# Kernel tuning notes

Hardware: AMD Instinct MI355X
Metric: run time of the kernel (lower is better)

Reference implementation:

```python
import jax, jax.numpy as jnp
import numpy as np

NUM_HEADS = 12
HEAD_CH = 64
WINDOW = 4


def _relative_to_absolute(x):
    # x: (B, H, L, 2L-1) -> (B, H, L, L) via skew trick
    B, H, L, _ = x.shape
    x = jnp.pad(x, ((0, 0), (0, 0), (0, 0), (0, 1)))        # (B,H,L,2L)
    x = x.reshape(B, H, L * 2 * L)
    x = jnp.pad(x, ((0, 0), (0, 0), (0, L - 1)))
    x = x.reshape(B, H, L + 1, 2 * L - 1)
    return x[:, :, :L, L - 1:]


def _get_relative_embeddings(emb, L):
    # emb: (H, 2W+1, D) -> (H, 2L-1, D)
    pad = max(0, L - WINDOW - 1)
    start = max(0, WINDOW - L + 1)
    e = jnp.pad(emb, ((0, 0), (pad, pad), (0, 0)))
    return e[:, start:start + 2 * L - 1, :]


def _forward(x, wq, bq, wk, bk, wv, bv, wo, bo, emb_rel_k, emb_rel_v):
    B, C, L = x.shape
    H, D = NUM_HEADS, HEAD_CH
    scale = 1.0 / np.sqrt(D).astype(np.float32)

    # 1x1 conv == channel matmul
    q = jnp.einsum('oc,bcl->bol', wq, x) + bq[None, :, None]
    k = jnp.einsum('oc,bcl->bol', wk, x) + bk[None, :, None]
    v = jnp.einsum('oc,bcl->bol', wv, x) + bv[None, :, None]

    # (B, C, L) -> (B, H, L, D)
    q = q.reshape(B, H, D, L).transpose(0, 1, 3, 2)
    k = k.reshape(B, H, D, L).transpose(0, 1, 3, 2)
    v = v.reshape(B, H, D, L).transpose(0, 1, 3, 2)

    score = jnp.einsum('bhld,bhmd->bhlm', q, k) * scale      # (B,H,L,L)

    rel_k = _get_relative_embeddings(emb_rel_k, L)           # (H, 2L-1, D)
    s_rel = jnp.einsum('bhld,hmd->bhlm', q, rel_k)           # (B,H,L,2L-1)
    score = score + _relative_to_absolute(s_rel) * scale

    attn = jax.nn.softmax(score, axis=-1)                    # dropout p=0 -> identity

    res = jnp.einsum('bhlm,bhmd->bhld', attn, v)             # (B,H,L,D)

    # absolute_to_relative skew
    a = jnp.pad(attn, ((0, 0), (0, 0), (0, 0), (0, L - 1)))
    a = a.reshape(B, H, L * (2 * L - 1))
    a = jnp.pad(a, ((0, 0), (0, 0), (L, 0)))
    rel_w = a.reshape(B, H, L, 2 * L)[:, :, :, 1:]           # (B,H,L,2L-1)

    rel_v = _get_relative_embeddings(emb_rel_v, L)           # (H, 2L-1, D)
    res = res + jnp.einsum('bhlm,hmd->bhld', rel_w, rel_v)

    res = res.transpose(0, 1, 3, 2).reshape(B, H * D, L)     # (B, C, L)
    out = jnp.einsum('oc,bcl->bol', wo, res) + bo[None, :, None]
    return out


def setup_inputs() -> dict:
    key = jax.random.key(0)
    ks = jax.random.split(key, 11)
    B, C, L = 4, 768, 1024
    rel_std = HEAD_CH ** (-0.5)
    xavier = np.sqrt(6.0 / (C + C)).astype(np.float32)
    return {
        'x': jax.random.normal(ks[0], (B, C, L), jnp.float32),
        'wq': jax.random.uniform(ks[1], (C, C), jnp.float32, -xavier, xavier),
        'bq': jnp.zeros((C,), jnp.float32),
        'wk': jax.random.uniform(ks[2], (C, C), jnp.float32, -xavier, xavier),
        'bk': jnp.zeros((C,), jnp.float32),
        'wv': jax.random.uniform(ks[3], (C, C), jnp.float32, -xavier, xavier),
        'bv': jnp.zeros((C,), jnp.float32),
        'wo': jax.random.normal(ks[4], (C, C), jnp.float32) * 0.02,
        'bo': jnp.zeros((C,), jnp.float32),
        'emb_rel_k': jax.random.normal(ks[5], (NUM_HEADS, 2 * WINDOW + 1, HEAD_CH), jnp.float32) * rel_std,
        'emb_rel_v': jax.random.normal(ks[6], (NUM_HEADS, 2 * WINDOW + 1, HEAD_CH), jnp.float32) * rel_std,
    }


def reference(x, wq, bq, wk, bk, wv, bv, wo, bo, emb_rel_k, emb_rel_v):
    return _forward(x, wq, bq, wk, bk, wv, bv, wo, bo, emb_rel_k, emb_rel_v)
```

## Files before the change

kernel.cpp:

```cpp
#include <hip/hip_runtime.h>

#define NB   4
#define NH   12
#define HD   64
#define CCH  768
#define LQ   1024
#define SCALE 0.125f
#define STAB  4.0f
#define WELE (CCH*CCH)

typedef unsigned short u16;
typedef __bf16 bf16x8 __attribute__((ext_vector_type(8)));
typedef unsigned short u16x8 __attribute__((ext_vector_type(8)));
typedef unsigned short u16x4 __attribute__((ext_vector_type(4)));
typedef float floatx4 __attribute__((ext_vector_type(4)));
typedef float floatx16 __attribute__((ext_vector_type(16)));

__device__ __forceinline__ float bf2f(u16 u) {
    union { unsigned int i; float f; } x; x.i = ((unsigned int)u) << 16; return x.f;
}
__device__ __forceinline__ u16 f2bf_u(float f) {
    union { float f; unsigned int i; } x; x.f = f;
    unsigned int i = x.i;
    return (u16)((i + 0x7FFFu + ((i >> 16) & 1u)) >> 16);
}
__device__ __forceinline__ void glds16(const u16* g, u16* l) {
    __builtin_amdgcn_global_load_lds(
        (const __attribute__((address_space(1))) unsigned int*)g,
        (__attribute__((address_space(3))) unsigned int*)l, 16, 0, 0);
}

__global__ __launch_bounds__(256) void convert_w_kernel(
    const float* __restrict__ wq, const float* __restrict__ wk,
    const float* __restrict__ wv, const float* __restrict__ wo,
    u16* __restrict__ wb)
{
    const int p = blockIdx.y;
    const float* src = (p == 0) ? wq : (p == 1) ? wk : (p == 2) ? wv : wo;
    u16* dst = wb + (size_t)p * WELE;
    const int idx = (blockIdx.x * 256 + threadIdx.x) * 4;
    const float4 v = *reinterpret_cast<const float4*>(src + idx);
    u16x4 o;
    o[0] = f2bf_u(v.x); o[1] = f2bf_u(v.y); o[2] = f2bf_u(v.z); o[3] = f2bf_u(v.w);
    *reinterpret_cast<u16x4*>(dst + idx) = o;
}

__global__ __launch_bounds__(256) void transpose_x_kernel(
    const float* __restrict__ x, u16* __restrict__ xT)
{
    __shared__ u16 tile[64 * 68];
    const int l0 = blockIdx.x * 64, c0 = blockIdx.y * 64, b = blockIdx.z;
    const int t = threadIdx.x;
    const float* xb = x + (size_t)b * CCH * LQ;
    {
        const int l = t & 63, cg = t >> 6;
        for (int i = 0; i < 16; ++i) {
            const int c = cg * 16 + i;
            tile[c * 68 + l] = f2bf_u(xb[(size_t)(c0 + c) * LQ + l0 + l]);
        }
    }
    __syncthreads();
    {
        const int c = t & 63, lg = t >> 6;
        for (int i = 0; i < 16; ++i) {
            const int l = lg * 16 + i;
            xT[((size_t)b * LQ + l0 + l) * CCH + c0 + c] = tile[c * 68 + l];
        }
    }
}

#define GEMM_CORE(Ag, Bg)                                                     \
    __shared__ __align__(16) u16 a_tile[128 * 64];                            \
    __shared__ __align__(16) u16 b_tile[128 * 64];                            \
    const int t = threadIdx.x;                                                \
    const int wave = t >> 6, lane = t & 63;                                   \
    const int quad = lane >> 4, l16 = lane & 15;                              \
    const int wm = (wave >> 1) * 64, wn = (wave & 1) * 64;                    \
    floatx4 acc[4][4];                                                        \
    _Pragma("unroll") for (int mi = 0; mi < 4; ++mi)                          \
        _Pragma("unroll") for (int ni = 0; ni < 4; ++ni)                      \
            _Pragma("unroll") for (int r = 0; r < 4; ++r) acc[mi][ni][r] = 0.f;\
    for (int k0 = 0; k0 < CCH; k0 += 64) {                                    \
        __syncthreads();                                                      \
        _Pragma("unroll") for (int i = 0; i < 4; ++i) {                       \
            const int sbase = wave * 256 + i * 64;                            \
            const int s = sbase + lane;                                       \
            const int m = s >> 3, pos = s & 7;                                \
            const int gpos = pos ^ (m & 7);                                   \
            glds16(Ag + (size_t)(m0 + m) * CCH + k0 + gpos * 8,               \
                   &a_tile[sbase * 8]);                                       \
            glds16(Bg + (size_t)(n0 + m) * CCH + k0 + gpos * 8,               \
                   &b_tile[sbase * 8]);                                       \
        }                                                                     \
        __syncthreads();                                                      \
        bf16x8 af[2][4], bfr[2][4];                                           \
        _Pragma("unroll") for (int s = 0; s < 2; ++s)                         \
            _Pragma("unroll") for (int i = 0; i < 4; ++i) {                   \
                const int am = wm + i * 16 + l16;                             \
                const int bn = wn + i * 16 + l16;                             \
                const int c = s * 4 + quad;                                   \
                af[s][i]  = *reinterpret_cast<const bf16x8*>(                 \
                    &a_tile[(am * 8 + (c ^ (am & 7))) * 8]);                  \
                bfr[s][i] = *reinterpret_cast<const bf16x8*>(                 \
                    &b_tile[(bn * 8 + (c ^ (bn & 7))) * 8]);                  \
            }                                                                 \
        _Pragma("unroll") for (int s = 0; s < 2; ++s)                         \
            _Pragma("unroll") for (int mi = 0; mi < 4; ++mi)                  \
                _Pragma("unroll") for (int ni = 0; ni < 4; ++ni)              \
                    acc[mi][ni] = __builtin_amdgcn_mfma_f32_16x16x32_bf16(    \
                        af[s][mi], bfr[s][ni], acc[mi][ni], 0, 0, 0);         \
    }

__global__ __launch_bounds__(256) void proj_qk_kernel(
    const u16* __restrict__ xT, const u16* __restrict__ wb,
    const float* __restrict__ bq, const float* __restrict__ bk,
    u16* __restrict__ Qlc, u16* __restrict__ Klc)
{
    const int z = blockIdx.z, b = z >> 1, p = z & 1;
    const int n0 = blockIdx.x * 128, m0 = blockIdx.y * 128;
    const u16* Ag = xT + (size_t)b * LQ * CCH;
    const u16* Bg = wb + (size_t)p * WELE;
    const float* bias = (p == 0) ? bq : bk;
    u16* Y = ((p == 0) ? Qlc : Klc) + (size_t)b * LQ * CCH;

    GEMM_CORE(Ag, Bg)

#pragma unroll
    for (int ni = 0; ni < 4; ++ni) {
        const int o = n0 + wn + ni * 16 + l16;
        const float bb = bias[o];
#pragma unroll
        for (int mi = 0; mi < 4; ++mi)
#pragma unroll
            for (int r = 0; r < 4; ++r) {
                const int l = m0 + wm + mi * 16 + quad * 4 + r;
                Y[(size_t)l * CCH + o] = f2bf_u(acc[mi][ni][r] + bb);
            }
    }
}

__global__ __launch_bounds__(256) void proj_v_kernel(
    const u16* __restrict__ xT, const u16* __restrict__ wb,
    const float* __restrict__ bv, u16* __restrict__ Vw)
{
    const int b = blockIdx.z;
    const int n0 = blockIdx.x * 128, m0 = blockIdx.y * 128;
    const u16* Ag = wb + (size_t)2 * WELE;
    const u16* Bg = xT + (size_t)b * LQ * CCH;
    u16* Y = Vw + (size_t)b * CCH * LQ;

    GEMM_CORE(Ag, Bg)

#pragma unroll
    for (int mi = 0; mi < 4; ++mi) {
#pragma unroll
        for (int r = 0; r < 4; ++r) {
            const int o = m0 + wm + mi * 16 + quad * 4 + r;
            const float bb = bv[o];
#pragma unroll
            for (int ni = 0; ni < 4; ++ni) {
                const int l = n0 + wn + ni * 16 + l16;
                Y[(size_t)o * LQ + l] = f2bf_u(acc[mi][ni][r] + bb);
            }
        }
    }
}

__global__ __launch_bounds__(256) void proj_out_kernel(
    const u16* __restrict__ resb, const u16* __restrict__ wb,
    const float* __restrict__ bo, float* __restrict__ out)
{
    const int b = blockIdx.z;
    const int n0 = blockIdx.x * 128, m0 = blockIdx.y * 128;
    const u16* Ag = wb + (size_t)3 * WELE;
    const u16* Bg = resb + (size_t)b * LQ * CCH;
    float* Y = out + (size_t)b * CCH * LQ;

    GEMM_CORE(Ag, Bg)

#pragma unroll
    for (int mi = 0; mi < 4; ++mi) {
#pragma unroll
        for (int r = 0; r < 4; ++r) {
            const int o = m0 + wm + mi * 16 + quad * 4 + r;
            const float bb = bo[o];
#pragma unroll
            for (int ni = 0; ni < 4; ++ni) {
                const int l = n0 + wn + ni * 16 + l16;
                Y[(size_t)o * LQ + l] = acc[mi][ni][r] + bb;
            }
        }
    }
}

#define KSTRIDE 72
#define PSTR 40

__global__ __launch_bounds__(256) void attn_kernel(
    const u16* __restrict__ Qlc, const u16* __restrict__ Klc,
    const u16* __restrict__ Vw,
    const float* __restrict__ erk, const float* __restrict__ erv,
    u16* __restrict__ resb)
{
    __shared__ __align__(16) u16 kv_lds[2 * 64 * KSTRIDE];
    __shared__ __align__(16) u16 p_lds[4 * 32 * PSTR];
    __shared__ float bias_lds[64 * 9];
    __shared__ float bandw_lds[64 * 9];
    __shared__ float erk_lds[9 * 64];
    __shared__ float erv_lds[9 * 64];
    __shared__ float l_red[64];

    u16* k16 = kv_lds;
    u16* v16 = kv_lds + 64 * KSTRIDE;
    float* ored = (float*)kv_lds;
    u16* kdiag = kv_lds;

    const int t = threadIdx.x;
    const int wave = t >> 6, lane = t & 63;
    const int hw = lane >> 5, l32 = lane & 31;
    const int qh = wave & 1, kh = wave >> 1;
    const int l0 = blockIdx.x * 64, h = blockIdx.y, b = blockIdx.z;

    const u16* Qb = Qlc + (size_t)b * LQ * CCH + h * HD;
    const u16* Kb = Klc + (size_t)b * LQ * CCH + h * HD;
    const u16* Vb = Vw + ((size_t)b * CCH + h * HD) * LQ;

    for (int i = t; i < 9 * 64; i += 256) {
        erk_lds[i] = erk[(size_t)h * 9 * 64 + i];
        erv_lds[i] = erv[(size_t)h * 9 * 64 + i];
    }

    const int qrow = qh * 32 + l32;
    const int lgq = l0 + qrow;

    bf16x8 qa[4];
#pragma unroll
    for (int c = 0; c < 4; ++c)
        qa[c] = *reinterpret_cast<const bf16x8*>(&Qb[(size_t)lgq * CCH + c * 16 + hw * 8]);

    __syncthreads();

    if (kh == 0) {
        float qf[32];
#pragma unroll
        for (int c = 0; c < 4; ++c) {
            union { bf16x8 v; u16x8 u; } a; a.v = qa[c];
#pragma unroll
            for (int j = 0; j < 8; ++j) qf[c * 8 + j] = bf2f(a.u[j]);
        }
        for (int dl = 0; dl < 9; ++dl) {
            float s = 0.f;
#pragma unroll
            for (int c = 0; c < 4; ++c)
#pragma unroll
                for (int j = 0; j < 8; ++j)
                    s += qf[c * 8 + j] * erk_lds[dl * 64 + c * 16 + hw * 8 + j];
            s += __shfl_xor(s, 32, 64);
            if (hw == 0) bias_lds[qrow * 9 + dl] = s;
        }
    }

    floatx16 O[2];
#pragma unroll
    for (int dt = 0; dt < 2; ++dt)
#pragma unroll
        for (int r = 0; r < 16; ++r) O[dt][r] = 0.f;
    float l_acc = 0.f;

    u16* pw = p_lds + wave * 32 * PSTR;

    for (int kb = 0; kb < 16; ++kb) {
        const int j0 = kb * 64;
        __syncthreads();
        {
            const int j = t >> 2, seg = t & 3;
            const u16x8* ks = reinterpret_cast<const u16x8*>(&Kb[(size_t)(j0 + j) * CCH + seg * 16]);
            *reinterpret_cast<u16x8*>(&k16[j * KSTRIDE + seg * 16])     = ks[0];
            *reinterpret_cast<u16x8*>(&k16[j * KSTRIDE + seg * 16 + 8]) = ks[1];
            const u16x8* vs = reinterpret_cast<const u16x8*>(&Vb[(size_t)j * LQ + j0 + seg * 16]);
            *reinterpret_cast<u16x8*>(&v16[j * KSTRIDE + seg * 16])     = vs[0];
            *reinterpret_cast<u16x8*>(&v16[j * KSTRIDE + seg * 16 + 8]) = vs[1];
        }
        __syncthreads();

        floatx16 sc;
#pragma unroll
        for (int r = 0; r < 16; ++r) sc[r] = 0.f;
#pragma unroll
        for (int c = 0; c < 4; ++c) {
            const bf16x8 ka = *reinterpret_cast<const bf16x8*>(
                &k16[(kh * 32 + l32) * KSTRIDE + c * 16 + hw * 8]);
            sc = __builtin_amdgcn_mfma_f32_32x32x16_bf16(ka, qa[c], sc, 0, 0, 0);
        }

        const int kbase = j0 + kh * 32;
        if (kbase + 31 >= l0 + qh * 32 - 4 && kbase <= l0 + qh * 32 + 35) {
#pragma unroll
            for (int r = 0; r < 16; ++r) {
                const int key = kbase + (r & 3) + 8 * (r >> 2) + 4 * hw;
                const int delta = key - lgq + 4;
                if (delta >= 0 && delta <= 8) sc[r] += bias_lds[qrow * 9 + delta];
            }
        }

        u16 pk[16];
#pragma unroll
        for (int r = 0; r < 16; ++r) {
            const float p = __expf(fmaf(sc[r], SCALE, -STAB));
            l_acc += p;
            pk[r] = f2bf_u(p);
        }
#pragma unroll
        for (int g = 0; g < 4; ++g)
            *reinterpret_cast<u16x4*>(&pw[l32 * PSTR + 8 * g + 4 * hw]) =
                *reinterpret_cast<const u16x4*>(&pk[4 * g]);

#pragma unroll
        for (int c2 = 0; c2 < 2; ++c2) {
            const bf16x8 pa = *reinterpret_cast<const bf16x8*>(
                &pw[l32 * PSTR + c2 * 16 + hw * 8]);
#pragma unroll
            for (int dt = 0; dt < 2; ++dt) {
                const bf16x8 vb = *reinterpret_cast<const bf16x8*>(
                    &v16[(dt * 32 + l32) * KSTRIDE + kh * 32 + c2 * 16 + hw * 8]);
                O[dt] = __builtin_amdgcn_mfma_f32_32x32x16_bf16(pa, vb, O[dt], 0, 0, 0);
            }
        }
    }

    l_acc += __shfl_xor(l_acc, 32, 64);

    __syncthreads();
    if (kh == 1) {
        if (hw == 0) l_red[qrow] = l_acc;
#pragma unroll
        for (int dt = 0; dt < 2; ++dt)
#pragma unroll
            for (int r = 0; r < 16; ++r) {
                const int row = (r & 3) + 8 * (r >> 2) + 4 * hw;
                ored[(qh * 32 + row) * 64 + dt * 32 + l32] = O[dt][r];
            }
    }
    __syncthreads();
    if (kh == 0) {
        const float linv = 1.0f / (l_acc + l_red[qrow]);
#pragma unroll
        for (int dt = 0; dt < 2; ++dt)
#pragma unroll
            for (int r = 0; r < 16; ++r) {
                const int row = (r & 3) + 8 * (r >> 2) + 4 * hw;
                O[dt][r] += ored[(qh * 32 + row) * 64 + dt * 32 + l32];
            }
        if (hw == 0) l_red[qrow] = linv;
    }
    __syncthreads();

    {
        const int i0 = t >> 2, seg = t & 3;
        const int jc = min(max(l0 - 4 + i0, 0), LQ - 1);
        const u16x8* s0 = reinterpret_cast<const u16x8*>(&Kb[(size_t)jc * CCH + seg * 16]);
        *reinterpret_cast<u16x8*>(&kdiag[i0 * KSTRIDE + seg * 16])     = s0[0];
        *reinterpret_cast<u16x8*>(&kdiag[i0 * KSTRIDE + seg * 16 + 8]) = s0[1];
        if (t < 32) {
            const int i1 = 64 + (t >> 2);
            const int j2 = min(l0 - 4 + i1, LQ - 1);
            const u16x8* s1 = reinterpret_cast<const u16x8*>(&Kb[(size_t)j2 * CCH + seg * 16]);
            *reinterpret_cast<u16x8*>(&kdiag[i1 * KSTRIDE + seg * 16])     = s1[0];
            *reinterpret_cast<u16x8*>(&kdiag[i1 * KSTRIDE + seg * 16 + 8]) = s1[1];
        }
    }
    __syncthreads();

    if (kh == 0) {
        float qf[32];
#pragma unroll
        for (int c = 0; c < 4; ++c) {
            union { bf16x8 v; u16x8 u; } a; a.v = qa[c];
#pragma unroll
            for (int j = 0; j < 8; ++j) qf[c * 8 + j] = bf2f(a.u[j]);
        }
        for (int dl = 0; dl < 9; ++dl) {
            const int i = qrow + dl;
            float s = 0.f;
#pragma unroll
            for (int c = 0; c < 4; ++c) {
                union { bf16x8 v; u16x8 u; } kd;
                kd.v = *reinterpret_cast<const bf16x8*>(&kdiag[i * KSTRIDE + c * 16 + hw * 8]);
#pragma unroll
                for (int j = 0; j < 8; ++j) s += qf[c * 8 + j] * bf2f(kd.u[j]);
            }
            s += __shfl_xor(s, 32, 64);
            const int jgl = lgq + dl - 4;
            float pband = 0.f;
            if (jgl >= 0 && jgl < LQ)
                pband = __expf(fmaf(s + bias_lds[qrow * 9 + dl], SCALE, -STAB));
            if (hw == 0) bandw_lds[qrow * 9 + dl] = pband;
        }

#pragma unroll
        for (int dt = 0; dt < 2; ++dt) {
#pragma unroll
            for (int r = 0; r < 16; ++r) {
                const int row = (r & 3) + 8 * (r >> 2) + 4 * hw;
                const int d = dt * 32 + l32;
                float val = O[dt][r];
#pragma unroll
                for (int dl = 0; dl < 9; ++dl)
                    val += bandw_lds[(qh * 32 + row) * 9 + dl] * erv_lds[dl * 64 + d];
                val *= l_red[qh * 32 + row];
                resb[((size_t)b * LQ + l0 + qh * 32 + row) * CCH + h * HD + d] = f2bf_u(val);
            }
        }
    }
}

extern "C" void kernel_launch(void* const* d_in, const int* in_sizes, int n_in,
                              void* d_out, int out_size, void* d_ws, size_t ws_size,
                              hipStream_t stream) {
    const float* x   = (const float*)d_in[0];
    const float* wq  = (const float*)d_in[1];
    const float* bq  = (const float*)d_in[2];
    const float* wk  = (const float*)d_in[3];
    const float* bk  = (const float*)d_in[4];
    const float* wv  = (const float*)d_in[5];
    const float* bv  = (const float*)d_in[6];
    const float* wo  = (const float*)d_in[7];
    const float* bo  = (const float*)d_in[8];
    const float* erk = (const float*)d_in[9];
    const float* erv = (const float*)d_in[10];
    float* out = (float*)d_out;

    const size_t NEL = (size_t)NB * CCH * LQ;
    u16* xT   = (u16*)d_ws;
    u16* wb   = xT + NEL;
    u16* Qlc  = wb + (size_t)4 * WELE;
    u16* Klc  = Qlc + NEL;
    u16* Vw   = Klc + NEL;
    u16* resb = Vw + NEL;

    convert_w_kernel<<<dim3(WELE / 1024, 4), 256, 0, stream>>>(wq, wk, wv, wo, wb);
    transpose_x_kernel<<<dim3(16, 12, 4), 256, 0, stream>>>(x, xT);
    proj_qk_kernel<<<dim3(6, 8, 8), 256, 0, stream>>>(xT, wb, bq, bk, Qlc, Klc);
    proj_v_kernel<<<dim3(8, 6, 4), 256, 0, stream>>>(xT, wb, bv, Vw);
    attn_kernel<<<dim3(LQ / 64, NH, NB), 256, 0, stream>>>(
        Qlc, Klc, Vw, erk, erv, resb);
    proj_out_kernel<<<dim3(8, 6, 4), 256, 0, stream>>>(resb, wb, bo, out);
}
```

Measured before the change: 202.1 us.

## Merge prep and QKV launches, restructure attention to two waves per block

Fuses the weight conversion and x transpose into one launch, and the Q/K and V projections into one launch, cutting launch count and letting the blocks share the GPU. The attention kernel moves from four waves splitting keys across two halves to two waves that each process all 64 keys of a tile. This removes the cross-wave reduction of O and l through shared memory and its extra barriers. In exchange each block has half the threads for loads and more serial MFMA work per wave, which may lower occupancy-driven latency hiding.

```diff
diff --git a/kernel.cpp b/kernel.cpp
--- a/kernel.cpp
+++ b/kernel.cpp
@@ -1,4 +1,5 @@
 #include <hip/hip_runtime.h>
+#include <hip/hip_bf16.h>
 
 #define NB   4
 #define NH   12
@@ -24,48 +25,56 @@
     unsigned int i = x.i;
     return (u16)((i + 0x7FFFu + ((i >> 16) & 1u)) >> 16);
 }
+__device__ __forceinline__ u16x4 f2bf4(float a, float b, float c, float d) {
+    union { __hip_bfloat162 h2[2]; u16x4 v; } p;
+    p.h2[0] = __float22bfloat162_rn(make_float2(a, b));
+    p.h2[1] = __float22bfloat162_rn(make_float2(c, d));
+    return p.v;
+}
 __device__ __forceinline__ void glds16(const u16* g, u16* l) {
     __builtin_amdgcn_global_load_lds(
         (const __attribute__((address_space(1))) unsigned int*)g,
         (__attribute__((address_space(3))) unsigned int*)l, 16, 0, 0);
 }
 
-__global__ __launch_bounds__(256) void convert_w_kernel(
+__global__ __launch_bounds__(256) void prep_kernel(
+    const float* __restrict__ x,
     const float* __restrict__ wq, const float* __restrict__ wk,
     const float* __restrict__ wv, const float* __restrict__ wo,
-    u16* __restrict__ wb)
-{
-    const int p = blockIdx.y;
-    const float* src = (p == 0) ? wq : (p == 1) ? wk : (p == 2) ? wv : wo;
-    u16* dst = wb + (size_t)p * WELE;
-    const int idx = (blockIdx.x * 256 + threadIdx.x) * 4;
-    const float4 v = *reinterpret_cast<const float4*>(src + idx);
-    u16x4 o;
-    o[0] = f2bf_u(v.x); o[1] = f2bf_u(v.y); o[2] = f2bf_u(v.z); o[3] = f2bf_u(v.w);
-    *reinterpret_cast<u16x4*>(dst + idx) = o;
-}
-
-__global__ __launch_bounds__(256) void transpose_x_kernel(
-    const float* __restrict__ x, u16* __restrict__ xT)
+    u16* __restrict__ wb, u16* __restrict__ xT)
 {
     __shared__ u16 tile[64 * 68];
-    const int l0 = blockIdx.x * 64, c0 = blockIdx.y * 64, b = blockIdx.z;
+    const int idx = blockIdx.x;
     const int t = threadIdx.x;
-    const float* xb = x + (size_t)b * CCH * LQ;
-    {
-        const int l = t & 63, cg = t >> 6;
-        for (int i = 0; i < 16; ++i) {
-            const int c = cg * 16 + i;
-            tile[c * 68 + l] = f2bf_u(xb[(size_t)(c0 + c) * LQ + l0 + l]);
-        }
-    }
-    __syncthreads();
-    {
-        const int c = t & 63, lg = t >> 6;
-        for (int i = 0; i < 16; ++i) {
-            const int l = lg * 16 + i;
-            xT[((size_t)b * LQ + l0 + l) * CCH + c0 + c] = tile[c * 68 + l];
-        }
+    if (idx < 768) {
+        const int b = idx / 192, rem = idx % 192;
+        const int c0 = (rem / 16) * 64, l0 = (rem % 16) * 64;
+        const float* xb = x + (size_t)b * CCH * LQ;
+        {
+            const int l = t & 63, cg = t >> 6;
+            for (int i = 0; i < 16; ++i) {
+                const int c = cg * 16 + i;
+                tile[c * 68 + l] = f2bf_u(xb[(size_t)(c0 + c) * LQ + l0 + l]);
+            }
+        }
+        __syncthreads();
+        {
+            const int c = t & 63, lg = t >> 6;
+            for (int i = 0; i < 16; ++i) {
+                const int l = lg * 16 + i;
+                xT[((size_t)b * LQ + l0 + l) * CCH + c0 + c] = tile[c * 68 + l];
+            }
+        }
+    } else {
+        const int j = idx - 768;
+        const int p = j / 576, blk = j % 576;
+        const float* src = (p == 0) ? wq : (p == 1) ? wk : (p == 2) ? wv : wo;
+        u16* dst = wb + (size_t)p * WELE;
+        const int i4 = (blk * 256 + t) * 4;
+        const float4 v = *reinterpret_cast<const float4*>(src + i4);
+        u16x4 o;
+        o[0] = f2bf_u(v.x); o[1] = f2bf_u(v.y); o[2] = f2bf_u(v.z); o[3] = f2bf_u(v.w);
+        *reinterpret_cast<u16x4*>(dst + i4) = o;
     }
 }
 
@@ -111,56 +120,62 @@
                         af[s][mi], bfr[s][ni], acc[mi][ni], 0, 0, 0);         \
     }
 
-__global__ __launch_bounds__(256) void proj_qk_kernel(
+__global__ __launch_bounds__(256) void proj_qkv_kernel(
     const u16* __restrict__ xT, const u16* __restrict__ wb,
     const float* __restrict__ bq, const float* __restrict__ bk,
-    u16* __restrict__ Qlc, u16* __restrict__ Klc)
+    const float* __restrict__ bv,
+    u16* __restrict__ Qlc, u16* __restrict__ Klc, u16* __restrict__ Vw)
 {
-    const int z = blockIdx.z, b = z >> 1, p = z & 1;
-    const int n0 = blockIdx.x * 128, m0 = blockIdx.y * 128;
-    const u16* Ag = xT + (size_t)b * LQ * CCH;
-    const u16* Bg = wb + (size_t)p * WELE;
-    const float* bias = (p == 0) ? bq : bk;
-    u16* Y = ((p == 0) ? Qlc : Klc) + (size_t)b * LQ * CCH;
+    const int b = blockIdx.y;
+    const int idx = blockIdx.x;
+    const bool qk = idx < 96;
+    const u16* Ag; const u16* Bg; int m0, n0, p;
+    if (qk) {
+        p = idx / 48;
+        const int r48 = idx % 48;
+        m0 = (r48 / 6) * 128;
+        n0 = p * 768 + (r48 % 6) * 128;
+        Ag = xT + (size_t)b * LQ * CCH;
+        Bg = wb;
+    } else {
+        const int vi = idx - 96;
+        m0 = 2 * 768 + (vi / 8) * 128;
+        n0 = (vi % 8) * 128;
+        Ag = wb;
+        Bg = xT + (size_t)b * LQ * CCH;
+        p = 2;
+    }
 
     GEMM_CORE(Ag, Bg)
 
-#pragma unroll
-    for (int ni = 0; ni < 4; ++ni) {
-        const int o = n0 + wn + ni * 16 + l16;
-        const float bb = bias[o];
-#pragma unroll
-        for (int mi = 0; mi < 4; ++mi)
+    if (qk) {
+        u16* Y = ((p == 0) ? Qlc : Klc) + (size_t)b * LQ * CCH;
+        const float* bias = (p == 0) ? bq : bk;
+#pragma unroll
+        for (int ni = 0; ni < 4; ++ni) {
+            const int o = (n0 - p * 768) + wn + ni * 16 + l16;
+            const float bb = bias[o];
+#pragma unroll
+            for (int mi = 0; mi < 4; ++mi)
+#pragma unroll
+                for (int r = 0; r < 4; ++r) {
+                    const int l = m0 + wm + mi * 16 + quad * 4 + r;
+                    Y[(size_t)l * CCH + o] = f2bf_u(acc[mi][ni][r] + bb);
+                }
+        }
+    } else {
+        u16* Y = Vw + (size_t)b * CCH * LQ;
+#pragma unroll
+        for (int mi = 0; mi < 4; ++mi) {
 #pragma unroll
             for (int r = 0; r < 4; ++r) {
-                const int l = m0 + wm + mi * 16 + quad * 4 + r;
-                Y[(size_t)l * CCH + o] = f2bf_u(acc[mi][ni][r] + bb);
-            }
-    }
-}
-
-__global__ __launch_bounds__(256) void proj_v_kernel(
-    const u16* __restrict__ xT, const u16* __restrict__ wb,
-    const float* __restrict__ bv, u16* __restrict__ Vw)
-{
-    const int b = blockIdx.z;
-    const int n0 = blockIdx.x * 128, m0 = blockIdx.y * 128;
-    const u16* Ag = wb + (size_t)2 * WELE;
-    const u16* Bg = xT + (size_t)b * LQ * CCH;
-    u16* Y = Vw + (size_t)b * CCH * LQ;
-
-    GEMM_CORE(Ag, Bg)
-
-#pragma unroll
-    for (int mi = 0; mi < 4; ++mi) {
-#pragma unroll
-        for (int r = 0; r < 4; ++r) {
-            const int o = m0 + wm + mi * 16 + quad * 4 + r;
-            const float bb = bv[o];
-#pragma unroll
-            for (int ni = 0; ni < 4; ++ni) {
-                const int l = n0 + wn + ni * 16 + l16;
-                Y[(size_t)o * LQ + l] = f2bf_u(acc[mi][ni][r] + bb);
+                const int o = (m0 - 1536) + wm + mi * 16 + quad * 4 + r;
+                const float bb = bv[o];
+#pragma unroll
+                for (int ni = 0; ni < 4; ++ni) {
+                    const int l = n0 + wn + ni * 16 + l16;
+                    Y[(size_t)o * LQ + l] = f2bf_u(acc[mi][ni][r] + bb);
+                }
             }
         }
     }
@@ -194,16 +209,16 @@
 }
 
 #define KSTRIDE 72
-#define PSTR 40
-
-__global__ __launch_bounds__(256) void attn_kernel(
+#define PSTR 72
+
+__global__ __launch_bounds__(128) void attn_kernel(
     const u16* __restrict__ Qlc, const u16* __restrict__ Klc,
     const u16* __restrict__ Vw,
     const float* __restrict__ erk, const float* __restrict__ erv,
     u16* __restrict__ resb)
 {
     __shared__ __align__(16) u16 kv_lds[2 * 64 * KSTRIDE];
-    __shared__ __align__(16) u16 p_lds[4 * 32 * PSTR];
+    __shared__ __align__(16) u16 p_lds[2 * 32 * PSTR];
     __shared__ float bias_lds[64 * 9];
     __shared__ float bandw_lds[64 * 9];
     __shared__ float erk_lds[9 * 64];
@@ -212,25 +227,23 @@
 
     u16* k16 = kv_lds;
     u16* v16 = kv_lds + 64 * KSTRIDE;
-    float* ored = (float*)kv_lds;
     u16* kdiag = kv_lds;
 
     const int t = threadIdx.x;
     const int wave = t >> 6, lane = t & 63;
     const int hw = lane >> 5, l32 = lane & 31;
-    const int qh = wave & 1, kh = wave >> 1;
     const int l0 = blockIdx.x * 64, h = blockIdx.y, b = blockIdx.z;
 
     const u16* Qb = Qlc + (size_t)b * LQ * CCH + h * HD;
     const u16* Kb = Klc + (size_t)b * LQ * CCH + h * HD;
     const u16* Vb = Vw + ((size_t)b * CCH + h * HD) * LQ;
 
-    for (int i = t; i < 9 * 64; i += 256) {
+    for (int i = t; i < 9 * 64; i += 128) {
         erk_lds[i] = erk[(size_t)h * 9 * 64 + i];
         erv_lds[i] = erv[(size_t)h * 9 * 64 + i];
     }
 
-    const int qrow = qh * 32 + l32;
+    const int qrow = wave * 32 + l32;
     const int lgq = l0 + qrow;
 
     bf16x8 qa[4];
@@ -240,7 +253,7 @@
 
     __syncthreads();
 
-    if (kh == 0) {
+    {
         float qf[32];
 #pragma unroll
         for (int c = 0; c < 4; ++c) {
@@ -268,110 +281,96 @@
     float l_acc = 0.f;
 
     u16* pw = p_lds + wave * 32 * PSTR;
+    const int l0w = l0 + wave * 32;
 
     for (int kb = 0; kb < 16; ++kb) {
         const int j0 = kb * 64;
         __syncthreads();
         {
-            const int j = t >> 2, seg = t & 3;
-            const u16x8* ks = reinterpret_cast<const u16x8*>(&Kb[(size_t)(j0 + j) * CCH + seg * 16]);
-            *reinterpret_cast<u16x8*>(&k16[j * KSTRIDE + seg * 16])     = ks[0];
-            *reinterpret_cast<u16x8*>(&k16[j * KSTRIDE + seg * 16 + 8]) = ks[1];
-            const u16x8* vs = reinterpret_cast<const u16x8*>(&Vb[(size_t)j * LQ + j0 + seg * 16]);
-            *reinterpret_cast<u16x8*>(&v16[j * KSTRIDE + seg * 16])     = vs[0];
-            *reinterpret_cast<u16x8*>(&v16[j * KSTRIDE + seg * 16 + 8]) = vs[1];
+            const int row = t >> 1, seg = (t & 1) * 32;
+            const u16x8* ks = reinterpret_cast<const u16x8*>(&Kb[(size_t)(j0 + row) * CCH + seg]);
+            u16x8* kd = reinterpret_cast<u16x8*>(&k16[row * KSTRIDE + seg]);
+            kd[0] = ks[0]; kd[1] = ks[1]; kd[2] = ks[2]; kd[3] = ks[3];
+            const u16x8* vs = reinterpret_cast<const u16x8*>(&Vb[(size_t)row * LQ + j0 + seg]);
+            u16x8* vd = reinterpret_cast<u16x8*>(&v16[row * KSTRIDE + seg]);
+            vd[0] = vs[0]; vd[1] = vs[1]; vd[2] = vs[2]; vd[3] = vs[3];
         }
         __syncthreads();
 
-        floatx16 sc;
-#pragma unroll
-        for (int r = 0; r < 16; ++r) sc[r] = 0.f;
+        floatx16 sc[2];
+#pragma unroll
+        for (int kt = 0; kt < 2; ++kt) {
+#pragma unroll
+            for (int r = 0; r < 16; ++r) sc[kt][r] = 0.f;
+#pragma unroll
+            for (int c = 0; c < 4; ++c) {
+                const bf16x8 ka = *reinterpret_cast<const bf16x8*>(
+                    &k16[(kt * 32 + l32) * KSTRIDE + c * 16 + hw * 8]);
+                sc[kt] = __builtin_amdgcn_mfma_f32_32x32x16_bf16(ka, qa[c], sc[kt], 0, 0, 0);
+            }
+        }
+
+        if (j0 + 63 >= l0w - 4 && j0 <= l0w + 35) {
+#pragma unroll
+            for (int kt = 0; kt < 2; ++kt)
+#pragma unroll
+                for (int r = 0; r < 16; ++r) {
+                    const int key = j0 + kt * 32 + (r & 3) + 8 * (r >> 2) + 4 * hw;
+                    const int delta = key - lgq + 4;
+                    if (delta >= 0 && delta <= 8) sc[kt][r] += bias_lds[qrow * 9 + delta];
+                }
+        }
+
+#pragma unroll
+        for (int kt = 0; kt < 2; ++kt) {
+#pragma unroll
+            for (int g = 0; g < 4; ++g) {
+                float pv[4];
+#pragma unroll
+                for (int q4 = 0; q4 < 4; ++q4) {
+                    pv[q4] = __expf(fmaf(sc[kt][g * 4 + q4], SCALE, -STAB));
+                    l_acc += pv[q4];
+                }
+                *reinterpret_cast<u16x4*>(&pw[l32 * PSTR + kt * 32 + 8 * g + 4 * hw]) =
+                    f2bf4(pv[0], pv[1], pv[2], pv[3]);
+            }
+        }
+
 #pragma unroll
         for (int c = 0; c < 4; ++c) {
-            const bf16x8 ka = *reinterpret_cast<const bf16x8*>(
-                &k16[(kh * 32 + l32) * KSTRIDE + c * 16 + hw * 8]);
-            sc = __builtin_amdgcn_mfma_f32_32x32x16_bf16(ka, qa[c], sc, 0, 0, 0);
-        }
-
-        const int kbase = j0 + kh * 32;
-        if (kbase + 31 >= l0 + qh * 32 - 4 && kbase <= l0 + qh * 32 + 35) {
-#pragma unroll
-            for (int r = 0; r < 16; ++r) {
-                const int key = kbase + (r & 3) + 8 * (r >> 2) + 4 * hw;
-                const int delta = key - lgq + 4;
-                if (delta >= 0 && delta <= 8) sc[r] += bias_lds[qrow * 9 + delta];
-            }
-        }
-
-        u16 pk[16];
-#pragma unroll
-        for (int r = 0; r < 16; ++r) {
-            const float p = __expf(fmaf(sc[r], SCALE, -STAB));
-            l_acc += p;
-            pk[r] = f2bf_u(p);
-        }
-#pragma unroll
-        for (int g = 0; g < 4; ++g)
-            *reinterpret_cast<u16x4*>(&pw[l32 * PSTR + 8 * g + 4 * hw]) =
-                *reinterpret_cast<const u16x4*>(&pk[4 * g]);
-
-#pragma unroll
-        for (int c2 = 0; c2 < 2; ++c2) {
             const bf16x8 pa = *reinterpret_cast<const bf16x8*>(
-                &pw[l32 * PSTR + c2 * 16 + hw * 8]);
+                &pw[l32 * PSTR + c * 16 + hw * 8]);
 #pragma unroll
             for (int dt = 0; dt < 2; ++dt) {
                 const bf16x8 vb = *reinterpret_cast<const bf16x8*>(
-                    &v16[(dt * 32 + l32) * KSTRIDE + kh * 32 + c2 * 16 + hw * 8]);
+                    &v16[(dt * 32 + l32) * KSTRIDE + c * 16 + hw * 8]);
                 O[dt] = __builtin_amdgcn_mfma_f32_32x32x16_bf16(pa, vb, O[dt], 0, 0, 0);
             }
         }
     }
 
     l_acc += __shfl_xor(l_acc, 32, 64);
+    if (hw == 0) l_red[qrow] = 1.0f / l_acc;
 
     __syncthreads();
-    if (kh == 1) {
-        if (hw == 0) l_red[qrow] = l_acc;
-#pragma unroll
-        for (int dt = 0; dt < 2; ++dt)
-#pragma unroll
-            for (int r = 0; r < 16; ++r) {
-                const int row = (r & 3) + 8 * (r >> 2) + 4 * hw;
-                ored[(qh * 32 + row) * 64 + dt * 32 + l32] = O[dt][r];
-            }
+
+    {
+        const int row = t >> 1, seg = (t & 1) * 32;
+        const int jc = min(max(l0 - 4 + row, 0), LQ - 1);
+        const u16x8* s0 = reinterpret_cast<const u16x8*>(&Kb[(size_t)jc * CCH + seg]);
+        u16x8* d0 = reinterpret_cast<u16x8*>(&kdiag[row * KSTRIDE + seg]);
+        d0[0] = s0[0]; d0[1] = s0[1]; d0[2] = s0[2]; d0[3] = s0[3];
+        if (t < 16) {
+            const int row2 = 64 + (t >> 1);
+            const int j2 = min(l0 - 4 + row2, LQ - 1);
+            const u16x8* s1 = reinterpret_cast<const u16x8*>(&Kb[(size_t)j2 * CCH + seg]);
+            u16x8* d1 = reinterpret_cast<u16x8*>(&kdiag[row2 * KSTRIDE + seg]);
+            d1[0] = s1[0]; d1[1] = s1[1]; d1[2] = s1[2]; d1[3] = s1[3];
+        }
     }
     __syncthreads();
-    if (kh == 0) {
-        const float linv = 1.0f / (l_acc + l_red[qrow]);
-#pragma unroll
-        for (int dt = 0; dt < 2; ++dt)
-#pragma unroll
-            for (int r = 0; r < 16; ++r) {
-                const int row = (r & 3) + 8 * (r >> 2) + 4 * hw;
-                O[dt][r] += ored[(qh * 32 + row) * 64 + dt * 32 + l32];
-            }
-        if (hw == 0) l_red[qrow] = linv;
-    }
-    __syncthreads();
 
     {
-        const int i0 = t >> 2, seg = t & 3;
-        const int jc = min(max(l0 - 4 + i0, 0), LQ - 1);
-        const u16x8* s0 = reinterpret_cast<const u16x8*>(&Kb[(size_t)jc * CCH + seg * 16]);
-        *reinterpret_cast<u16x8*>(&kdiag[i0 * KSTRIDE + seg * 16])     = s0[0];
-        *reinterpret_cast<u16x8*>(&kdiag[i0 * KSTRIDE + seg * 16 + 8]) = s0[1];
-        if (t < 32) {
-            const int i1 = 64 + (t >> 2);
-            const int j2 = min(l0 - 4 + i1, LQ - 1);
-            const u16x8* s1 = reinterpret_cast<const u16x8*>(&Kb[(size_t)j2 * CCH + seg * 16]);
-            *reinterpret_cast<u16x8*>(&kdiag[i1 * KSTRIDE + seg * 16])     = s1[0];
-            *reinterpret_cast<u16x8*>(&kdiag[i1 * KSTRIDE + seg * 16 + 8]) = s1[1];
-        }
-    }
-    __syncthreads();
-
-    if (kh == 0) {
         float qf[32];
 #pragma unroll
         for (int c = 0; c < 4; ++c) {
@@ -396,20 +395,21 @@
                 pband = __expf(fmaf(s + bias_lds[qrow * 9 + dl], SCALE, -STAB));
             if (hw == 0) bandw_lds[qrow * 9 + dl] = pband;
         }
-
-#pragma unroll
-        for (int dt = 0; dt < 2; ++dt) {
-#pragma unroll
-            for (int r = 0; r < 16; ++r) {
-                const int row = (r & 3) + 8 * (r >> 2) + 4 * hw;
-                const int d = dt * 32 + l32;
-                float val = O[dt][r];
-#pragma unroll
-                for (int dl = 0; dl < 9; ++dl)
-                    val += bandw_lds[(qh * 32 + row) * 9 + dl] * erv_lds[dl * 64 + d];
-                val *= l_red[qh * 32 + row];
-                resb[((size_t)b * LQ + l0 + qh * 32 + row) * CCH + h * HD + d] = f2bf_u(val);
-            }
+    }
+
+#pragma unroll
+    for (int dt = 0; dt < 2; ++dt) {
+#pragma unroll
+        for (int r = 0; r < 16; ++r) {
+            const int row = (r & 3) + 8 * (r >> 2) + 4 * hw;
+            const int qg = wave * 32 + row;
+            const int d = dt * 32 + l32;
+            float val = O[dt][r];
+#pragma unroll
+            for (int dl = 0; dl < 9; ++dl)
+                val += bandw_lds[qg * 9 + dl] * erv_lds[dl * 64 + d];
+            val *= l_red[qg];
+            resb[((size_t)b * LQ + l0 + qg) * CCH + h * HD + d] = f2bf_u(val);
         }
     }
 }
@@ -438,11 +438,10 @@
     u16* Vw   = Klc + NEL;
     u16* resb = Vw + NEL;
 
-    convert_w_kernel<<<dim3(WELE / 1024, 4), 256, 0, stream>>>(wq, wk, wv, wo, wb);
-    transpose_x_kernel<<<dim3(16, 12, 4), 256, 0, stream>>>(x, xT);
-    proj_qk_kernel<<<dim3(6, 8, 8), 256, 0, stream>>>(xT, wb, bq, bk, Qlc, Klc);
-    proj_v_kernel<<<dim3(8, 6, 4), 256, 0, stream>>>(xT, wb, bv, Vw);
-    attn_kernel<<<dim3(LQ / 64, NH, NB), 256, 0, stream>>>(
+    prep_kernel<<<dim3(768 + 4 * 576), 256, 0, stream>>>(x, wq, wk, wv, wo, wb, xT);
+    proj_qkv_kernel<<<dim3(144, 4), 256, 0, stream>>>(
+        xT, wb, bq, bk, bv, Qlc, Klc, Vw);
+    attn_kernel<<<dim3(LQ / 64, NH, NB), 128, 0, stream>>>(
         Qlc, Klc, Vw, erk, erv, resb);
     proj_out_kernel<<<dim3(8, 6, 4), 256, 0, stream>>>(resb, wb, bo, out);
 }
```

Measured after the change: 204.4 us. No clear change (+1.1%).
